# Kernel optimization log

Measured on AMD Instinct MI355X. Metric: run time of the kernel, lower is better.

## Reference

```python
import jax, jax.numpy as jnp
import numpy as np

N, D = 2048, 64


def setup_inputs() -> dict:
    key = jax.random.key(0)
    y_samples = jax.random.normal(key, (N, D), dtype=jnp.float32)
    return {"y_samples": y_samples}


def reference(y_samples) -> jnp.ndarray:
    # mi_est_org (CLUB upper bound, non-variational):
    #   positive = 0
    #   negative[i, d] = -mean_j (y[j, d] - y[i, d])^2 / 2
    #   upper_bound = mean_i ( 0 - sum_d negative[i, d] )
    # prediction_1 = y[:, None, :]  (i axis), y_samples_1 = y[None, :, :] (j axis)
    diff = y_samples[None, :, :] - y_samples[:, None, :]          # [i=N, j=N, D]
    negative = -jnp.mean(diff * diff, axis=1) / 2.0               # mean over j -> [N, D]
    upper_bound = jnp.mean(-jnp.sum(negative, axis=-1))           # scalar
    return upper_bound
```

## Files before the change

kernel.cpp:

```cpp
#include <hip/hip_runtime.h>


#define N_ROWS 2048
#define D_COLS 64
#define NBLK 64
#define NTHR 256
#define ROWS_PER_BLOCK (N_ROWS / NBLK)
#define FLAG_MAGIC 0x5AC0FFEE0DDBA11ULL


__global__ __launch_bounds__(NTHR)
void mi_fused(const float* __restrict__ y, float* __restrict__ ws,
              float* __restrict__ out) {
    __shared__ float s1s[NTHR];
    __shared__ float s2s[NTHR];
    unsigned long long* flags = (unsigned long long*)(ws + NBLK * 128);

    const int t    = threadIdx.x;
    const int b    = blockIdx.x;
    const int col  = t & 63;
    const int rsub = t >> 6;
    const int rowBase = b * ROWS_PER_BLOCK;

    float s1 = 0.0f, s2 = 0.0f;
    #pragma unroll
    for (int k = 0; k < ROWS_PER_BLOCK / 4; ++k) {
        const float v = y[(rowBase + rsub + 4 * k) * D_COLS + col];
        s1 += v;
        s2 += v * v;
    }
    s1s[t] = s1;
    s2s[t] = s2;
    __syncthreads();

    if (t < 64) {
        const float a1 = s1s[t] + s1s[t + 64] + s1s[t + 128] + s1s[t + 192];
        const float a2 = s2s[t] + s2s[t + 64] + s2s[t + 128] + s2s[t + 192];
        ws[b * 128 + t]      = a1;
        ws[b * 128 + 64 + t] = a2;
    }
    if (t == 0)
        __hip_atomic_store(&flags[b], FLAG_MAGIC, __ATOMIC_RELEASE,
                           __HIP_MEMORY_SCOPE_AGENT);

    if (b != 0) return;

    if (t < 64) {
        while (__hip_atomic_load(&flags[t], __ATOMIC_ACQUIRE,
                                 __HIP_MEMORY_SCOPE_AGENT) != FLAG_MAGIC) { }
        __hip_atomic_store(&flags[t], 0ULL, __ATOMIC_RELAXED,
                           __HIP_MEMORY_SCOPE_AGENT);
    }
    __syncthreads();

    const int grp = t >> 6;
    float S1 = 0.0f, S2 = 0.0f;
    #pragma unroll
    for (int k = 0; k < 16; ++k) {
        const int bb = grp * 16 + k;
        S1 += __hip_atomic_load(&ws[bb * 128 + col], __ATOMIC_RELAXED,
                                __HIP_MEMORY_SCOPE_AGENT);
        S2 += __hip_atomic_load(&ws[bb * 128 + 64 + col], __ATOMIC_RELAXED,
                                __HIP_MEMORY_SCOPE_AGENT);
    }
    s1s[t] = S1;
    s2s[t] = S2;
    __syncthreads();

    if (t < 64) {
        const float T1 = s1s[t] + s1s[t + 64] + s1s[t + 128] + s1s[t + 192];
        const float T2 = s2s[t] + s2s[t + 64] + s2s[t + 128] + s2s[t + 192];
        const float invN = 1.0f / (float)N_ROWS;
        float v = T2 * invN - (T1 * invN) * (T1 * invN);
        #pragma unroll
        for (int off = 32; off > 0; off >>= 1)
            v += __shfl_down(v, off);
        if (t == 0) out[0] = v;
    }
}

extern "C" void kernel_launch(void* const* d_in, const int* in_sizes, int n_in,
                              void* d_out, int out_size, void* d_ws, size_t ws_size,
                              hipStream_t stream) {
    const float* y = (const float*)d_in[0];
    float* out = (float*)d_out;
    float* ws  = (float*)d_ws;

    mi_fused<<<NBLK, NTHR, 0, stream>>>(y, ws, out);
}
```

Baseline: 9.488 us.

## Halve grid to 32 blocks with float4 loads and coalesced final reduction

Measured after the change: 11.70 us. 23.3% more time.

```diff
diff --git a/kernel.cpp b/kernel.cpp
--- a/kernel.cpp
+++ b/kernel.cpp
@@ -1,43 +1,44 @@
 #include <hip/hip_runtime.h>
 
 
-#define N_ROWS 2048
-#define D_COLS 64
-#define NBLK 64
 #define NTHR 256
-#define ROWS_PER_BLOCK (N_ROWS / NBLK)
-#define FLAG_MAGIC 0x5AC0FFEE0DDBA11ULL
+#define NBLK 32
+#define FLAG_MAGIC 0x5AC0FFEE00DDBA11ULL
 
 
 __global__ __launch_bounds__(NTHR)
 void mi_fused(const float* __restrict__ y, float* __restrict__ ws,
               float* __restrict__ out) {
-    __shared__ float s1s[NTHR];
-    __shared__ float s2s[NTHR];
+    __shared__ float4 l1[NTHR];
+    __shared__ float4 l2[NTHR];
+    __shared__ float  sm[NTHR];
     unsigned long long* flags = (unsigned long long*)(ws + NBLK * 128);
+    const int t = threadIdx.x;
+    const int b = blockIdx.x;
 
-    const int t    = threadIdx.x;
-    const int b    = blockIdx.x;
-    const int col  = t & 63;
-    const int rsub = t >> 6;
-    const int rowBase = b * ROWS_PER_BLOCK;
-
-    float s1 = 0.0f, s2 = 0.0f;
+    const float4* y4 = (const float4*)y + (size_t)b * 1024;
+    float4 a1 = make_float4(0.f, 0.f, 0.f, 0.f);
+    float4 a2 = make_float4(0.f, 0.f, 0.f, 0.f);
     #pragma unroll
-    for (int k = 0; k < ROWS_PER_BLOCK / 4; ++k) {
-        const float v = y[(rowBase + rsub + 4 * k) * D_COLS + col];
-        s1 += v;
-        s2 += v * v;
+    for (int k = 0; k < 4; ++k) {
+        const float4 v = y4[t + NTHR * k];
+        a1.x += v.x;     a1.y += v.y;     a1.z += v.z;     a1.w += v.w;
+        a2.x += v.x*v.x; a2.y += v.y*v.y; a2.z += v.z*v.z; a2.w += v.w*v.w;
     }
-    s1s[t] = s1;
-    s2s[t] = s2;
+    l1[t] = a1;
+    l2[t] = a2;
     __syncthreads();
 
     if (t < 64) {
-        const float a1 = s1s[t] + s1s[t + 64] + s1s[t + 128] + s1s[t + 192];
-        const float a2 = s2s[t] + s2s[t + 64] + s2s[t + 128] + s2s[t + 192];
-        ws[b * 128 + t]      = a1;
-        ws[b * 128 + 64 + t] = a2;
+        const int g = t >> 2, e = t & 3;
+        float s1 = 0.f, s2 = 0.f;
+        #pragma unroll
+        for (int j = 0; j < 16; ++j) {
+            s1 += ((const float*)&l1[16 * j + g])[e];
+            s2 += ((const float*)&l2[16 * j + g])[e];
+        }
+        ws[b * 128 + t]      = s1;
+        ws[b * 128 + 64 + t] = s2;
     }
     if (t == 0)
         __hip_atomic_store(&flags[b], FLAG_MAGIC, __ATOMIC_RELEASE,
@@ -45,33 +46,29 @@
 
     if (b != 0) return;
 
-    if (t < 64) {
-        while (__hip_atomic_load(&flags[t], __ATOMIC_ACQUIRE,
-                                 __HIP_MEMORY_SCOPE_AGENT) != FLAG_MAGIC) { }
+    if (t < NBLK) {
+        while (__hip_atomic_load(&flags[t], __ATOMIC_RELAXED,
+                                 __HIP_MEMORY_SCOPE_AGENT) != FLAG_MAGIC) {}
         __hip_atomic_store(&flags[t], 0ULL, __ATOMIC_RELAXED,
                            __HIP_MEMORY_SCOPE_AGENT);
     }
     __syncthreads();
+    __builtin_amdgcn_fence(__ATOMIC_ACQUIRE, "agent");
 
-    const int grp = t >> 6;
-    float S1 = 0.0f, S2 = 0.0f;
+    float p = 0.f;
     #pragma unroll
-    for (int k = 0; k < 16; ++k) {
-        const int bb = grp * 16 + k;
-        S1 += __hip_atomic_load(&ws[bb * 128 + col], __ATOMIC_RELAXED,
-                                __HIP_MEMORY_SCOPE_AGENT);
-        S2 += __hip_atomic_load(&ws[bb * 128 + 64 + col], __ATOMIC_RELAXED,
-                                __HIP_MEMORY_SCOPE_AGENT);
-    }
-    s1s[t] = S1;
-    s2s[t] = S2;
+    for (int k = 0; k < 16; ++k)
+        p += __hip_atomic_load(&ws[t + NTHR * k], __ATOMIC_RELAXED,
+                               __HIP_MEMORY_SCOPE_AGENT);
+    sm[t] = p;
     __syncthreads();
-
+    if (t < 128) sm[t] = sm[t] + sm[t + 128];
+    __syncthreads();
     if (t < 64) {
-        const float T1 = s1s[t] + s1s[t + 64] + s1s[t + 128] + s1s[t + 192];
-        const float T2 = s2s[t] + s2s[t + 64] + s2s[t + 128] + s2s[t + 192];
-        const float invN = 1.0f / (float)N_ROWS;
-        float v = T2 * invN - (T1 * invN) * (T1 * invN);
+        const float invN = 1.0f / 2048.0f;
+        const float S1 = sm[t];
+        const float S2 = sm[t + 64];
+        float v = S2 * invN - (S1 * invN) * (S1 * invN);
         #pragma unroll
         for (int off = 32; off > 0; off >>= 1)
             v += __shfl_down(v, off);
```
